# Optimization experiments

Hardware: AMD Instinct MI355X
Metric: run time of the kernel (lower is better)

Reference implementation:

```python
import jax, jax.numpy as jnp
import numpy as np

TOP_K = 2


def setup_inputs() -> dict:
    key = jax.random.key(0)
    k1, k2 = jax.random.split(key)
    x = jax.random.normal(k1, (4, 4096, 2048), dtype=jnp.float32)
    # router weight, init std=0.01 as in the module
    w_router = jax.random.normal(k2, (64, 2048), dtype=jnp.float32) * 0.01
    return {"x": x, "w_router": w_router}


def reference(x, w_router):
    B, S, D = x.shape
    E = w_router.shape[0]
    N = B * S  # num_tokens
    xt = x.reshape(N, D)
    # router linear (no bias, no jitter: eval mode / jitter=0)
    router_logits = jnp.einsum("nd,ed->ne", xt, w_router)  # [N, E]
    router_probs = jax.nn.softmax(router_logits, axis=-1)
    top_k_probs, top_k_indices = jax.lax.top_k(router_probs, TOP_K)  # [N, K]
    top_k_probs_norm = top_k_probs / jnp.sum(top_k_probs, axis=-1, keepdims=True)
    # load-balancing aux loss
    router_prob_per_expert = jnp.mean(router_probs, axis=0)  # [E]
    aux_loss = jnp.mean(E * router_prob_per_expert * router_prob_per_expert)
    # vectorized scatter replacing the python double-loop:
    # dispatch[token, expert] = normalized top-k prob
    token_idx = jnp.arange(N)[:, None]  # [N, 1] broadcasts over K
    dispatch_tensor = jnp.zeros((N, E), dtype=x.dtype).at[token_idx, top_k_indices].set(top_k_probs_norm)
    combine_tensor = dispatch_tensor
    return (dispatch_tensor, combine_tensor, router_logits, router_probs,
            aux_loss, top_k_indices, top_k_probs_norm)
```

## Files before the change

kernel.cpp:

```cpp
#include <hip/hip_runtime.h>

#define D_DIM 2048
#define E_DIM 64
#define BT 256
#define DSPLIT 4
#define DCH (D_DIM / DSPLIT)
#define DK 32
#define NTILE (DCH / DK)
#define XBYTES (BT * DK * 4)
#define WBYTES (E_DIM * DK * 4)
#define BUFB (XBYTES + WBYTES)

typedef __attribute__((address_space(3))) char as3_char;
typedef __attribute__((address_space(1))) const char as1_char;

__global__ __launch_bounds__(256, 1) void router_gemm(
    const float* __restrict__ x, const float* __restrict__ w,
    float* __restrict__ out, int N) {
  __shared__ __align__(16) char lds[2][BUFB];
  const int tid = threadIdx.x;
  const int l = tid & 63;
  const int wv = tid >> 6;
  const int tbase = blockIdx.x * BT;
  const int dbase = blockIdx.y * DCH;

  const int scol = ((l & 7) ^ (l >> 3)) * 4;
  const float* xsrc[8];
#pragma unroll
  for (int q = 0; q < 8; ++q) {
    int row = (wv * 8 + q) * 8 + (l >> 3);
    xsrc[q] = x + (size_t)(tbase + row) * D_DIM + dbase + scol;
  }
  const float* wsrc[2];
#pragma unroll
  for (int q = 0; q < 2; ++q) {
    int e = (wv * 2 + q) * 8 + (l >> 3);
    wsrc[q] = w + (size_t)e * D_DIM + dbase + scol;
  }

  auto STAGE = [&](int b, int t) {
    const int d0 = t * DK;
#pragma unroll
    for (int q = 0; q < 8; ++q)
      __builtin_amdgcn_global_load_lds((as1_char*)(const char*)(xsrc[q] + d0),
                                       (as3_char*)&lds[b][(wv * 8 + q) * 1024],
                                       16, 0, 0);
#pragma unroll
    for (int q = 0; q < 2; ++q)
      __builtin_amdgcn_global_load_lds(
          (as1_char*)(const char*)(wsrc[q] + d0),
          (as3_char*)&lds[b][XBYTES + (wv * 2 + q) * 1024], 16, 0, 0);
  };

  const int tg = tid & 31;
  const int eg = tid >> 5;
  int xoff[8], woff[8];
#pragma unroll
  for (int i = 0; i < 8; ++i) xoff[i] = (tg + 32 * i) * 128 + ((tg & 7) << 4);
#pragma unroll
  for (int j = 0; j < 8; ++j) woff[j] = XBYTES + (eg * 8 + j) * 128 + (j << 4);

  float acc[8][8];
#pragma unroll
  for (int i = 0; i < 8; ++i)
#pragma unroll
    for (int j = 0; j < 8; ++j) acc[i][j] = 0.f;

  STAGE(0, 0);
  asm volatile("s_waitcnt vmcnt(0)" ::: "memory");
  __syncthreads();

  int cur = 0;
  for (int t = 0; t < NTILE; ++t) {
    if (t + 1 < NTILE) STAGE(cur ^ 1, t + 1);
    const char* buf = lds[cur];
#pragma unroll
    for (int d4 = 0; d4 < 8; ++d4) {
      const int dx = d4 << 4;
      float4 xv[8], wvv[8];
#pragma unroll
      for (int i = 0; i < 8; ++i)
        xv[i] = *(const float4*)(buf + (xoff[i] ^ dx));
#pragma unroll
      for (int j = 0; j < 8; ++j)
        wvv[j] = *(const float4*)(buf + (woff[j] ^ dx));
#pragma unroll
      for (int i = 0; i < 8; ++i)
#pragma unroll
        for (int j = 0; j < 8; ++j) {
          acc[i][j] = fmaf(xv[i].x, wvv[j].x, acc[i][j]);
          acc[i][j] = fmaf(xv[i].y, wvv[j].y, acc[i][j]);
          acc[i][j] = fmaf(xv[i].z, wvv[j].z, acc[i][j]);
          acc[i][j] = fmaf(xv[i].w, wvv[j].w, acc[i][j]);
        }
    }
    asm volatile("s_waitcnt vmcnt(0)" ::: "memory");
    __syncthreads();
    cur ^= 1;
  }

  float* part = out + (size_t)blockIdx.y * ((size_t)N * E_DIM);
#pragma unroll
  for (int i = 0; i < 8; ++i) {
    size_t o = (size_t)(tbase + tg + 32 * i) * E_DIM + eg * 8;
    *(float4*)(part + o) = make_float4(acc[i][0], acc[i][1], acc[i][2], acc[i][3]);
    *(float4*)(part + o + 4) = make_float4(acc[i][4], acc[i][5], acc[i][6], acc[i][7]);
  }
}

__global__ __launch_bounds__(256) void postprocess(float* out, float* ws, int N) {
  const int lane = threadIdx.x & 63;
  const int wv = threadIdx.x >> 6;
  const size_t NE = (size_t)N * E_DIM;
  float* disp = out;
  float* comb = out + NE;
  float* logits_o = out + 2 * NE;
  float* probs_o = out + 3 * NE;
  float* idx_o = out + 4 * NE + 1;
  float* pn_o = out + 4 * NE + 1 + 2 * (size_t)N;

  float expsum = 0.f;
  const int t0 = blockIdx.x * 64 + wv * 16;
  for (int k = 0; k < 16; ++k) {
    const size_t t = (size_t)(t0 + k);
    const size_t o = t * E_DIM + lane;
    float lv = (disp[o] + comb[o]) + (logits_o[o] + probs_o[o]);
    logits_o[o] = lv;
    float m = lv;
#pragma unroll
    for (int off = 32; off; off >>= 1) m = fmaxf(m, __shfl_xor(m, off));
    float p = __expf(lv - m);
    float s = p;
#pragma unroll
    for (int off = 32; off; off >>= 1) s += __shfl_xor(s, off);
    float prob = p / s;
    probs_o[o] = prob;
    expsum += prob;

    unsigned long long key =
        ((unsigned long long)__float_as_uint(prob) << 32) | (unsigned)(63 - lane);
    unsigned long long k1 = key;
#pragma unroll
    for (int off = 32; off; off >>= 1) {
      unsigned long long v = __shfl_xor(k1, off);
      if (v > k1) k1 = v;
    }
    int i1 = 63 - (int)(k1 & 63);
    unsigned long long k2 = (lane == i1) ? 0ull : key;
#pragma unroll
    for (int off = 32; off; off >>= 1) {
      unsigned long long v = __shfl_xor(k2, off);
      if (v > k2) k2 = v;
    }
    int i2 = 63 - (int)(k2 & 63);
    float p1 = __uint_as_float((unsigned)(k1 >> 32));
    float p2 = __uint_as_float((unsigned)(k2 >> 32));
    float inv = 1.0f / (p1 + p2);
    float pn1 = p1 * inv, pn2 = p2 * inv;
    float dval = (lane == i1) ? pn1 : ((lane == i2) ? pn2 : 0.f);
    disp[o] = dval;
    comb[o] = dval;
    if (lane == 0) {
      idx_o[2 * t] = (float)i1;
      idx_o[2 * t + 1] = (float)i2;
      pn_o[2 * t] = pn1;
      pn_o[2 * t + 1] = pn2;
    }
  }

  __shared__ float aux_s[4][64];
  aux_s[wv][lane] = expsum;
  __syncthreads();
  if (threadIdx.x < 64) {
    float s = aux_s[0][threadIdx.x] + aux_s[1][threadIdx.x] +
              aux_s[2][threadIdx.x] + aux_s[3][threadIdx.x];
    ws[(size_t)blockIdx.x * 64 + threadIdx.x] = s;
  }
}

__global__ __launch_bounds__(256) void finalize_aux(const float* __restrict__ ws,
                                                    float* __restrict__ auxp,
                                                    int nblocks, int N) {
  __shared__ float red[256];
  const int e = threadIdx.x & 63;
  const int part = threadIdx.x >> 6;
  float s = 0.f;
  for (int b = part; b < nblocks; b += 4) s += ws[(size_t)b * 64 + e];
  red[threadIdx.x] = s;
  __syncthreads();
  if (threadIdx.x < 64) {
    float tot = red[e] + red[64 + e] + red[128 + e] + red[192 + e];
    float pb = tot / (float)N;
    float v = pb * pb;
#pragma unroll
    for (int off = 32; off; off >>= 1) v += __shfl_xor(v, off);
    if (threadIdx.x == 0) *auxp = v;
  }
}

extern "C" void kernel_launch(void* const* d_in, const int* in_sizes, int n_in,
                              void* d_out, int out_size, void* d_ws, size_t ws_size,
                              hipStream_t stream) {
  (void)n_in; (void)out_size; (void)ws_size;
  const float* x = (const float*)d_in[0];
  const float* w = (const float*)d_in[1];
  float* out = (float*)d_out;
  const int N = in_sizes[0] / D_DIM;
  const int npb = N / 64;

  dim3 gg(N / BT, DSPLIT);
  router_gemm<<<gg, dim3(256), 0, stream>>>(x, w, out, N);
  postprocess<<<dim3(npb), dim3(256), 0, stream>>>(out, (float*)d_ws, N);
  finalize_aux<<<dim3(1), dim3(256), 0, stream>>>((const float*)d_ws,
                                                  out + 4 * (size_t)N * E_DIM,
                                                  npb, N);
}
```

Measured before the change: 276.1 us.

## Deepen GEMM load pipeline to four LDS buffers with smaller K tiles

Halves the K-tile depth and moves from double-buffered to four-buffer LDS staging, keeping three tiles of async global-to-LDS loads in flight. Partial vmcnt waits replace full drains, so compute on one tile overlaps outstanding loads for later ones. The LDS swizzle and read offsets are rebuilt for the 64-byte rows. In exchange there are twice as many barriers per K and more complex wait-count bookkeeping. The narrower swizzle may also raise bank conflicts.

Measured after the change: 288.3 us. +4.4%, slower.

```diff
diff --git a/kernel.cpp b/kernel.cpp
--- a/kernel.cpp
+++ b/kernel.cpp
@@ -5,11 +5,12 @@
 #define BT 256
 #define DSPLIT 4
 #define DCH (D_DIM / DSPLIT)
-#define DK 32
+#define DK 16
 #define NTILE (DCH / DK)
-#define XBYTES (BT * DK * 4)
-#define WBYTES (E_DIM * DK * 4)
-#define BUFB (XBYTES + WBYTES)
+#define XB (BT * DK * 4)
+#define WB (E_DIM * DK * 4)
+#define BUFB (XB + WB)
+#define NBUF 4
 
 typedef __attribute__((address_space(3))) char as3_char;
 typedef __attribute__((address_space(1))) const char as1_char;
@@ -17,48 +18,44 @@
 __global__ __launch_bounds__(256, 1) void router_gemm(
     const float* __restrict__ x, const float* __restrict__ w,
     float* __restrict__ out, int N) {
-  __shared__ __align__(16) char lds[2][BUFB];
+  __shared__ __align__(16) char lds[NBUF][BUFB];
   const int tid = threadIdx.x;
   const int l = tid & 63;
   const int wv = tid >> 6;
   const int tbase = blockIdx.x * BT;
   const int dbase = blockIdx.y * DCH;
 
-  const int scol = ((l & 7) ^ (l >> 3)) * 4;
-  const float* xsrc[8];
-#pragma unroll
-  for (int q = 0; q < 8; ++q) {
-    int row = (wv * 8 + q) * 8 + (l >> 3);
+  const int scol = ((l & 3) ^ ((l >> 3) & 3)) * 4;
+  const float* xsrc[4];
+#pragma unroll
+  for (int q = 0; q < 4; ++q) {
+    int row = (wv * 4 + q) * 16 + (l >> 2);
     xsrc[q] = x + (size_t)(tbase + row) * D_DIM + dbase + scol;
   }
-  const float* wsrc[2];
-#pragma unroll
-  for (int q = 0; q < 2; ++q) {
-    int e = (wv * 2 + q) * 8 + (l >> 3);
-    wsrc[q] = w + (size_t)e * D_DIM + dbase + scol;
-  }
+  const float* wsrc = w + (size_t)(wv * 16 + (l >> 2)) * D_DIM + dbase + scol;
 
   auto STAGE = [&](int b, int t) {
     const int d0 = t * DK;
 #pragma unroll
-    for (int q = 0; q < 8; ++q)
+    for (int q = 0; q < 4; ++q)
       __builtin_amdgcn_global_load_lds((as1_char*)(const char*)(xsrc[q] + d0),
-                                       (as3_char*)&lds[b][(wv * 8 + q) * 1024],
+                                       (as3_char*)&lds[b][(wv * 4 + q) * 1024],
                                        16, 0, 0);
-#pragma unroll
-    for (int q = 0; q < 2; ++q)
-      __builtin_amdgcn_global_load_lds(
-          (as1_char*)(const char*)(wsrc[q] + d0),
-          (as3_char*)&lds[b][XBYTES + (wv * 2 + q) * 1024], 16, 0, 0);
+    __builtin_amdgcn_global_load_lds((as1_char*)(const char*)(wsrc + d0),
+                                     (as3_char*)&lds[b][XB + wv * 1024], 16, 0, 0);
   };
 
   const int tg = tid & 31;
   const int eg = tid >> 5;
   int xoff[8], woff[8];
 #pragma unroll
-  for (int i = 0; i < 8; ++i) xoff[i] = (tg + 32 * i) * 128 + ((tg & 7) << 4);
-#pragma unroll
-  for (int j = 0; j < 8; ++j) woff[j] = XBYTES + (eg * 8 + j) * 128 + (j << 4);
+  for (int i = 0; i < 8; ++i)
+    xoff[i] = (tg + 32 * i) * 64 + (((tg >> 1) & 3) << 4);
+#pragma unroll
+  for (int j = 0; j < 8; ++j) {
+    int e = eg * 8 + j;
+    woff[j] = XB + e * 64 + (((e >> 1) & 3) << 4);
+  }
 
   float acc[8][8];
 #pragma unroll
@@ -67,15 +64,24 @@
     for (int j = 0; j < 8; ++j) acc[i][j] = 0.f;
 
   STAGE(0, 0);
-  asm volatile("s_waitcnt vmcnt(0)" ::: "memory");
-  __syncthreads();
-
-  int cur = 0;
+  STAGE(1, 1);
+  STAGE(2, 2);
+
   for (int t = 0; t < NTILE; ++t) {
-    if (t + 1 < NTILE) STAGE(cur ^ 1, t + 1);
-    const char* buf = lds[cur];
-#pragma unroll
-    for (int d4 = 0; d4 < 8; ++d4) {
+    if (t + 2 < NTILE) {
+      asm volatile("s_waitcnt vmcnt(10)" ::: "memory");
+    } else if (t + 2 == NTILE) {
+      asm volatile("s_waitcnt vmcnt(5)" ::: "memory");
+    } else {
+      asm volatile("s_waitcnt vmcnt(0)" ::: "memory");
+    }
+    __builtin_amdgcn_s_barrier();
+    __builtin_amdgcn_sched_barrier(0);
+    if (t + 3 < NTILE) STAGE((t + 3) & 3, t + 3);
+
+    const char* buf = lds[t & 3];
+#pragma unroll
+    for (int d4 = 0; d4 < 4; ++d4) {
       const int dx = d4 << 4;
       float4 xv[8], wvv[8];
 #pragma unroll
@@ -94,9 +100,6 @@
           acc[i][j] = fmaf(xv[i].w, wvv[j].w, acc[i][j]);
         }
     }
-    asm volatile("s_waitcnt vmcnt(0)" ::: "memory");
-    __syncthreads();
-    cur ^= 1;
   }
 
   float* part = out + (size_t)blockIdx.y * ((size_t)N * E_DIM);
```
